# Kernel optimization log

Measured on AMD Instinct MI355X. Metric: run time of the kernel, lower is better.

## Reference

```python
import jax, jax.numpy as jnp
import numpy as np

N, K, D = 500_000, 256, 64  # points, prototypes, feature dim


def setup_inputs() -> dict:
    key = jax.random.key(0)
    kx, km = jax.random.split(key)
    X = jax.random.normal(kx, (N, D), dtype=jnp.float32)
    mus = jax.random.normal(km, (K, D), dtype=jnp.float32)
    return {"X": X, "mus": mus}


def reference(X, mus):
    # Faithful to vmap(lambda x: argmin(sum((mus - x)**2, axis=1)))(X),
    # but expressed with the Gram-matrix distance trick so the K*D broadcast
    # is a single GEMM instead of an O(N,K,D) elementwise intermediate.
    x_sq = jnp.sum(X * X, axis=1, keepdims=True)        # [N, 1]
    mu_sq = jnp.sum(mus * mus, axis=1)                  # [K]
    d2 = x_sq - 2.0 * (X @ mus.T) + mu_sq[None, :]      # [N, K] squared dists
    return jnp.argmin(d2, axis=1)                       # [N] int assignments
```

## Files before the change

### kernel.cpp

```cpp
#include <hip/hip_runtime.h>


#define DIM 64
#define NPROTO 256
#define NBLK 1024
#define MARGIN_ACC 0.017f

using f32x4 = __attribute__((ext_vector_type(4))) float;
using f16x8 = __attribute__((ext_vector_type(8))) _Float16;

__device__ __forceinline__ f16x8 cvt8(float4 a, float4 b) {
    f16x8 r;
    r[0] = (_Float16)a.x; r[1] = (_Float16)a.y;
    r[2] = (_Float16)a.z; r[3] = (_Float16)a.w;
    r[4] = (_Float16)b.x; r[5] = (_Float16)b.y;
    r[6] = (_Float16)b.z; r[7] = (_Float16)b.w;
    return r;
}

__device__ __forceinline__ void barrier_keep_vmcnt() {
    asm volatile("s_waitcnt lgkmcnt(0)" ::: "memory");
    __builtin_amdgcn_s_barrier();
    __builtin_amdgcn_sched_barrier(0);
}

#define PACK_TREE(acc, b1, b2)                                          \
    {                                                                   \
        float pv[4];                                                    \
        _Pragma("unroll")                                               \
        for (int r = 0; r < 4; ++r) {                                   \
            unsigned u = __float_as_uint(acc[r]);                       \
            u = (u & 0xFFFFFF00u) + (unsigned)(kofs - p * 16 - r);      \
            pv[r] = __uint_as_float(u);                                 \
        }                                                               \
        const float t1a = fmaxf(pv[0], pv[1]), t2a = fminf(pv[0], pv[1]);\
        const float t1b = fmaxf(pv[2], pv[3]), t2b = fminf(pv[2], pv[3]);\
        const float p1 = fmaxf(t1a, t1b);                               \
        const float p2 = fmaxf(fminf(t1a, t1b), fmaxf(t2a, t2b));       \
        const float nb2 = fmaxf(fminf(b1, p1), fmaxf(b2, p2));          \
        b1 = fmaxf(b1, p1);                                             \
        b2 = nb2;                                                       \
    }

__attribute__((amdgpu_waves_per_eu(2, 4)))
__global__ void __launch_bounds__(128)
argmin_mfma_kernel(const float* __restrict__ X,
                   const float* __restrict__ mus,
                   int* __restrict__ out,
                   unsigned* __restrict__ ws_count,
                   int* __restrict__ ws_list,
                   int use_list, int n) {
    __shared__ __align__(16) float s_seed[NPROTO];
    __shared__ uint2 s_pair[2][32];

    const int tid = threadIdx.x;
    const int w = tid >> 6;
    const int l = tid & 63;
    const int lp = l & 15;
    const int lg = l >> 4;

    f16x8 ah[8][2];
#pragma unroll
    for (int p = 0; p < 8; ++p) {
        const float* src = mus + (size_t)(w * 128 + p * 16 + lp) * DIM + lg * 8;
        const float4 a = *(const float4*)(src);
        const float4 b = *(const float4*)(src + 4);
        const float4 c = *(const float4*)(src + 32);
        const float4 d = *(const float4*)(src + 36);
        ah[p][0] = cvt8(a, b);
        ah[p][1] = cvt8(c, d);
        float s = 0.f;
        s = fmaf(a.x, a.x, fmaf(a.y, a.y, fmaf(a.z, a.z, fmaf(a.w, a.w, s))));
        s = fmaf(b.x, b.x, fmaf(b.y, b.y, fmaf(b.z, b.z, fmaf(b.w, b.w, s))));
        s = fmaf(c.x, c.x, fmaf(c.y, c.y, fmaf(c.z, c.z, fmaf(c.w, c.w, s))));
        s = fmaf(d.x, d.x, fmaf(d.y, d.y, fmaf(d.z, d.z, fmaf(d.w, d.w, s))));
        s += __shfl_xor(s, 16);
        s += __shfl_xor(s, 32);
        if (lg == 0) s_seed[w * 128 + p * 16 + lp] = -0.5f * s;
    }
    __syncthreads();

    const int ng2 = (n + 31) / 32;
    const int q = ng2 / NBLK, rr = ng2 % NBLK;
    const int bid = blockIdx.x;
    const int g0 = bid * q + (bid < rr ? bid : rr);
    const int cnt = q + (bid < rr ? 1 : 0);

    const int kofs = 255 - w * 128 - lg * 4;
    const int sbase = w * 128 + lg * 4;

    float4 xa0, xa1, xa2, xa3, xb0, xb1, xb2, xb3;
    if (cnt > 0) {
        int rA = g0 * 32 + lp;      rA = (rA < n) ? rA : (n - 1);
        int rB = g0 * 32 + 16 + lp; rB = (rB < n) ? rB : (n - 1);
        const float* pA = X + (size_t)rA * DIM + lg * 8;
        const float* pB = X + (size_t)rB * DIM + lg * 8;
        xa0 = *(const float4*)(pA);      xa1 = *(const float4*)(pA + 4);
        xa2 = *(const float4*)(pA + 32); xa3 = *(const float4*)(pA + 36);
        xb0 = *(const float4*)(pB);      xb1 = *(const float4*)(pB + 4);
        xb2 = *(const float4*)(pB + 32); xb3 = *(const float4*)(pB + 36);
    }

    for (int it = 0; it < cnt; ++it) {
        const int g = g0 + it;
        const int par = it & 1;
        const bool more = (it + 1 < cnt);

        const f16x8 bxA0 = cvt8(xa0, xa1), bxA1 = cvt8(xa2, xa3);
        const f16x8 bxB0 = cvt8(xb0, xb1), bxB1 = cvt8(xb2, xb3);

        if (more) {
            int rA = (g + 1) * 32 + lp;      rA = (rA < n) ? rA : (n - 1);
            int rB = (g + 1) * 32 + 16 + lp; rB = (rB < n) ? rB : (n - 1);
            const float* pA = X + (size_t)rA * DIM + lg * 8;
            const float* pB = X + (size_t)rB * DIM + lg * 8;
            xa0 = *(const float4*)(pA);      xa1 = *(const float4*)(pA + 4);
            xa2 = *(const float4*)(pA + 32); xa3 = *(const float4*)(pA + 36);
            xb0 = *(const float4*)(pB);      xb1 = *(const float4*)(pB + 4);
            xb2 = *(const float4*)(pB + 32); xb3 = *(const float4*)(pB + 36);
        }

        float b1A = -3.4e38f, b2A = -3.4e38f;
        float b1B = -3.4e38f, b2B = -3.4e38f;
#pragma unroll
        for (int p = 0; p < 8; ++p) {
            const f32x4 seed = *(const f32x4*)&s_seed[sbase + p * 16];
            f32x4 accA = __builtin_amdgcn_mfma_f32_16x16x32_f16(
                ah[p][0], bxA0, seed, 0, 0, 0);
            f32x4 accB = __builtin_amdgcn_mfma_f32_16x16x32_f16(
                ah[p][0], bxB0, seed, 0, 0, 0);
            accA = __builtin_amdgcn_mfma_f32_16x16x32_f16(ah[p][1], bxA1,
                                                          accA, 0, 0, 0);
            accB = __builtin_amdgcn_mfma_f32_16x16x32_f16(ah[p][1], bxB1,
                                                          accB, 0, 0, 0);
            PACK_TREE(accA, b1A, b2A)
            PACK_TREE(accB, b1B, b2B)
        }
#pragma unroll
        for (int m = 16; m <= 32; m <<= 1) {
            const float o1A = __shfl_xor(b1A, m), o2A = __shfl_xor(b2A, m);
            const float o1B = __shfl_xor(b1B, m), o2B = __shfl_xor(b2B, m);
            const float n2A = fmaxf(fminf(b1A, o1A), fmaxf(b2A, o2A));
            const float n2B = fmaxf(fminf(b1B, o1B), fmaxf(b2B, o2B));
            b1A = fmaxf(b1A, o1A); b2A = n2A;
            b1B = fmaxf(b1B, o1B); b2B = n2B;
        }
        if (w == 1 && l < 16) {
            s_pair[par][l] = make_uint2(__float_as_uint(b1A),
                                        __float_as_uint(b2A));
            s_pair[par][16 + l] = make_uint2(__float_as_uint(b1B),
                                             __float_as_uint(b2B));
        }
        barrier_keep_vmcnt();

        bool fl = false;
        const int i = g * 32 + l;
        if (w == 0 && l < 32 && i < n) {
            float f1 = (l < 16) ? b1A : b1B;
            float f2 = (l < 16) ? b2A : b2B;
            const uint2 o = s_pair[par][l];
            const float o1 = __uint_as_float(o.x), o2 = __uint_as_float(o.y);
            const float nb2 = fmaxf(fminf(f1, o1), fmaxf(f2, o2));
            f1 = fmaxf(f1, o1);
            f2 = nb2;
            const unsigned u1 = __float_as_uint(f1);
            const int k1 = 255 - (int)(u1 & 0xFFu);
            const float v1 = __uint_as_float(u1 & 0xFFFFFF00u);
            const float v2 =
                __uint_as_float(__float_as_uint(f2) & 0xFFFFFF00u);
            const bool close = (v1 - v2) < MARGIN_ACC;
            if (use_list) {
                out[i] = k1;
                fl = close;
            } else {
                out[i] = (int)((unsigned)k1 | (close ? 0x80000000u : 0u));
            }
        }
        if (use_list) {
            const unsigned long long mask = __ballot(fl);
            if (mask) {
                unsigned base = 0;
                if (l == 0)
                    base = atomicAdd(ws_count, (unsigned)__popcll(mask));
                base = __shfl(base, 0);
                if (fl)
                    ws_list[base + __popcll(mask & ((1ull << l) - 1))] = i;
            }
        }
    }
}

#define MSTRIDE 65

__global__ void __launch_bounds__(256)
fixup_lds_kernel(const float* __restrict__ X, const float* __restrict__ mus,
                 const unsigned* __restrict__ ws_count,
                 const int* __restrict__ ws_list, int* __restrict__ out) {
    __shared__ float s_mu[NPROTO * MSTRIDE];
    __shared__ float s_msq[NPROTO];

    const int tid = threadIdx.x;
    {
        const float4* mr = (const float4*)(mus + (size_t)tid * DIM);
        float q0 = 0.f, q1 = 0.f, q2 = 0.f, q3 = 0.f;
#pragma unroll
        for (int qq = 0; qq < 16; ++qq) {
            const float4 mv = mr[qq];
            const int base = tid * MSTRIDE + qq * 4;
            s_mu[base]     = mv.x;
            s_mu[base + 1] = mv.y;
            s_mu[base + 2] = mv.z;
            s_mu[base + 3] = mv.w;
            q0 = fmaf(mv.x, mv.x, q0);
            q1 = fmaf(mv.y, mv.y, q1);
            q2 = fmaf(mv.z, mv.z, q2);
            q3 = fmaf(mv.w, mv.w, q3);
        }
        s_msq[tid] = (q0 + q1) + (q2 + q3);
    }
    __syncthreads();

    const int l = tid & 63;
    const int gw = (int)((blockIdx.x * blockDim.x + tid) >> 6);
    const int NW = (int)((gridDim.x * blockDim.x) >> 6);
    const int nf = (int)*ws_count;

    for (int j = gw; j < nf; j += NW) {
        const int pt = ws_list[j];
        const float4* xr = (const float4*)(X + (size_t)pt * DIM);
        float4 xv[16];
        float a0 = 0.f, a1 = 0.f, a2 = 0.f, a3 = 0.f;
#pragma unroll
        for (int qq = 0; qq < 16; ++qq) {
            xv[qq] = xr[qq];
            a0 = fmaf(xv[qq].x, xv[qq].x, a0);
            a1 = fmaf(xv[qq].y, xv[qq].y, a1);
            a2 = fmaf(xv[qq].z, xv[qq].z, a2);
            a3 = fmaf(xv[qq].w, xv[qq].w, a3);
        }
        const float xsq = (a0 + a1) + (a2 + a3);
        float b1 = 3.4e38f;
        int k1 = 0;
#pragma unroll
        for (int e = 0; e < 4; ++e) {
            const int p = e * 64 + l;
            const float* mr = &s_mu[p * MSTRIDE];
            float d0 = 0.f, d1 = 0.f, d2 = 0.f, d3 = 0.f;
#pragma unroll
            for (int qq = 0; qq < 16; ++qq) {
                d0 = fmaf(mr[qq * 4],     xv[qq].x, d0);
                d1 = fmaf(mr[qq * 4 + 1], xv[qq].y, d1);
                d2 = fmaf(mr[qq * 4 + 2], xv[qq].z, d2);
                d3 = fmaf(mr[qq * 4 + 3], xv[qq].w, d3);
            }
            const float dot = (d0 + d1) + (d2 + d3);
            const float dd = (xsq - 2.0f * dot) + s_msq[p];
            if (dd < b1) { b1 = dd; k1 = p; }
        }
#pragma unroll
        for (int mm = 1; mm < 64; mm <<= 1) {
            const float ob = __shfl_xor(b1, mm);
            const int ok = __shfl_xor(k1, mm);
            if (ob < b1 || (ob == b1 && ok < k1)) { b1 = ob; k1 = ok; }
        }
        if (l == 0) out[pt] = k1;
    }
}

__device__ __forceinline__ int recompute_point(const float* __restrict__ X,
                                               const float* __restrict__ mus,
                                               int pt, int l) {
    const float4* xr = (const float4*)(X + (size_t)pt * DIM);
    float4 xv[16];
    float xa0 = 0.f, xa1 = 0.f, xa2 = 0.f, xa3 = 0.f;
#pragma unroll
    for (int qq = 0; qq < 16; ++qq) {
        xv[qq] = xr[qq];
        xa0 = fmaf(xv[qq].x, xv[qq].x, xa0);
        xa1 = fmaf(xv[qq].y, xv[qq].y, xa1);
        xa2 = fmaf(xv[qq].z, xv[qq].z, xa2);
        xa3 = fmaf(xv[qq].w, xv[qq].w, xa3);
    }
    const float xsq = (xa0 + xa1) + (xa2 + xa3);
    float b1 = 3.4e38f; int k1 = 0;
#pragma unroll
    for (int e = 0; e < 4; ++e) {
        const int p = l * 4 + e;
        const float4* mr = (const float4*)(mus + (size_t)p * DIM);
        float d0 = 0.f, d1 = 0.f, d2a = 0.f, d3 = 0.f;
        float q0 = 0.f, q1 = 0.f, q2 = 0.f, q3 = 0.f;
#pragma unroll
        for (int qq = 0; qq < 16; ++qq) {
            const float4 mv = mr[qq];
            d0 = fmaf(mv.x, xv[qq].x, d0);
            d1 = fmaf(mv.y, xv[qq].y, d1);
            d2a = fmaf(mv.z, xv[qq].z, d2a);
            d3 = fmaf(mv.w, xv[qq].w, d3);
            q0 = fmaf(mv.x, mv.x, q0);
            q1 = fmaf(mv.y, mv.y, q1);
            q2 = fmaf(mv.z, mv.z, q2);
            q3 = fmaf(mv.w, mv.w, q3);
        }
        const float dot = (d0 + d1) + (d2a + d3);
        const float msq = (q0 + q1) + (q2 + q3);
        const float dd = (xsq - 2.0f * dot) + msq;
        if (dd < b1) { b1 = dd; k1 = p; }
    }
#pragma unroll
    for (int mm = 1; mm < 64; mm <<= 1) {
        const float ob = __shfl_xor(b1, mm);
        const int ok = __shfl_xor(k1, mm);
        if (ob < b1 || (ob == b1 && ok < k1)) { b1 = ob; k1 = ok; }
    }
    return k1;
}

__global__ void __launch_bounds__(256)
fixup_scan_kernel(const float* __restrict__ X, const float* __restrict__ mus,
                  int* __restrict__ out, int n) {
    const int gw = (int)((blockIdx.x * blockDim.x + threadIdx.x) >> 6);
    const int l = threadIdx.x & 63;
    const int NW = (int)((gridDim.x * blockDim.x) >> 6);
    const int chunk = (n + NW - 1) / NW;
    const int base = gw * chunk;
    const int end = (base + chunk < n) ? (base + chunk) : n;
    for (int s = base; s < end; s += 64) {
        const int i = s + l;
        const int v = (i < end) ? out[i] : 0;
        const bool flg = (i < end) && ((unsigned)v & 0x80000000u);
        unsigned long long m = __ballot(flg);
        while (m) {
            const int src = (int)__ffsll((unsigned long long)m) - 1;
            m &= m - 1;
            const int pt = __shfl(i, src);
            const int k1 = recompute_point(X, mus, pt, l);
            if (l == 0) out[pt] = k1;
        }
    }
}

extern "C" void kernel_launch(void* const* d_in, const int* in_sizes, int n_in,
                              void* d_out, int out_size, void* d_ws, size_t ws_size,
                              hipStream_t stream) {
    const float* X = (const float*)d_in[0];
    const float* mus = (const float*)d_in[1];
    int* out = (int*)d_out;
    const int n = in_sizes[0] / DIM;

    unsigned* ws_count = (unsigned*)d_ws;
    int* ws_list = (int*)((char*)d_ws + 16);
    const int use_list = (ws_size >= 16 + (size_t)n * 4) ? 1 : 0;

    if (use_list) {
        hipMemsetAsync(d_ws, 0, 16, stream);
    }

    argmin_mfma_kernel<<<NBLK, 128, 0, stream>>>(X, mus, out, ws_count,
                                                 ws_list, use_list, n);
    if (use_list) {
        fixup_lds_kernel<<<512, 256, 0, stream>>>(X, mus, ws_count, ws_list,
                                                  out);
    } else {
        fixup_scan_kernel<<<512, 256, 0, stream>>>(X, mus, out, n);
    }
}
```

Before: 77.28 us.

## Unroll main loop by two with double-buffered X prefetch and drop atomic fixup list

```diff
diff --git a/kernel.cpp b/kernel.cpp
--- a/kernel.cpp
+++ b/kernel.cpp
@@ -42,16 +42,88 @@
         b2 = nb2;                                                       \
     }
 
+#define LOADX(gt, x0, x1, x2, x3, y0, y1, y2, y3)                       \
+    {                                                                   \
+        int rA_ = (gt) * 32 + lp;      rA_ = (rA_ < n) ? rA_ : (n - 1); \
+        int rB_ = (gt) * 32 + 16 + lp; rB_ = (rB_ < n) ? rB_ : (n - 1); \
+        const float* pA_ = X + (size_t)rA_ * DIM + lg * 8;              \
+        const float* pB_ = X + (size_t)rB_ * DIM + lg * 8;              \
+        x0 = *(const float4*)(pA_);      x1 = *(const float4*)(pA_ + 4);\
+        x2 = *(const float4*)(pA_ + 32); x3 = *(const float4*)(pA_ + 36);\
+        y0 = *(const float4*)(pB_);      y1 = *(const float4*)(pB_ + 4);\
+        y2 = *(const float4*)(pB_ + 32); y3 = *(const float4*)(pB_ + 36);\
+    }
+
+#define BODY(gcur, gnext, PAR, x0, x1, x2, x3, y0, y1, y2, y3)          \
+    {                                                                   \
+        const f16x8 bxA0 = cvt8(x0, x1), bxA1 = cvt8(x2, x3);           \
+        const f16x8 bxB0 = cvt8(y0, y1), bxB1 = cvt8(y2, y3);           \
+        LOADX(gnext, x0, x1, x2, x3, y0, y1, y2, y3)                    \
+        float b1A = -3.4e38f, b2A = -3.4e38f;                           \
+        float b1B = -3.4e38f, b2B = -3.4e38f;                           \
+        _Pragma("unroll")                                               \
+        for (int p = 0; p < 8; ++p) {                                   \
+            const f32x4 seed = *(const f32x4*)&s_seed[sbase + p * 16];  \
+            f32x4 accA = __builtin_amdgcn_mfma_f32_16x16x32_f16(        \
+                ah[p][0], bxA0, seed, 0, 0, 0);                         \
+            f32x4 accB = __builtin_amdgcn_mfma_f32_16x16x32_f16(        \
+                ah[p][0], bxB0, seed, 0, 0, 0);                         \
+            accA = __builtin_amdgcn_mfma_f32_16x16x32_f16(              \
+                ah[p][1], bxA1, accA, 0, 0, 0);                         \
+            accB = __builtin_amdgcn_mfma_f32_16x16x32_f16(              \
+                ah[p][1], bxB1, accB, 0, 0, 0);                         \
+            PACK_TREE(accA, b1A, b2A)                                   \
+            PACK_TREE(accB, b1B, b2B)                                   \
+        }                                                               \
+        _Pragma("unroll")                                               \
+        for (int m = 16; m <= 32; m <<= 1) {                            \
+            const float o1A = __shfl_xor(b1A, m), o2A = __shfl_xor(b2A, m);\
+            const float o1B = __shfl_xor(b1B, m), o2B = __shfl_xor(b2B, m);\
+            const float n2A = fmaxf(fminf(b1A, o1A), fmaxf(b2A, o2A));  \
+            const float n2B = fmaxf(fminf(b1B, o1B), fmaxf(b2B, o2B));  \
+            b1A = fmaxf(b1A, o1A); b2A = n2A;                           \
+            b1B = fmaxf(b1B, o1B); b2B = n2B;                           \
+        }                                                               \
+         \
+         \
+        if (w == 0 && l >= 16 && l < 32)                                \
+            s_pair[PAR][0][l] = make_uint2(__float_as_uint(b1B),        \
+                                           __float_as_uint(b2B));       \
+        if (w == 1 && l < 16)                                           \
+            s_pair[PAR][1][l] = make_uint2(__float_as_uint(b1A),        \
+                                           __float_as_uint(b2A));       \
+        barrier_keep_vmcnt();                                           \
+        const bool mine = (w == 0) ? (l < 16) : (l >= 16 && l < 32);    \
+        if (mine) {                                                     \
+            float f1 = (l < 16) ? b1A : b1B;                            \
+            float f2 = (l < 16) ? b2A : b2B;                            \
+            const uint2 o = s_pair[PAR][1 - w][l];                      \
+            const float o1 = __uint_as_float(o.x);                      \
+            const float o2 = __uint_as_float(o.y);                      \
+            const float nb2 = fmaxf(fminf(f1, o1), fmaxf(f2, o2));      \
+            f1 = fmaxf(f1, o1);                                         \
+            f2 = nb2;                                                   \
+            const int i = (gcur) * 32 + l;                              \
+            if (i < n) {                                                \
+                const unsigned u1 = __float_as_uint(f1);                \
+                const int k1 = 255 - (int)(u1 & 0xFFu);                 \
+                const float v1 = __uint_as_float(u1 & 0xFFFFFF00u);     \
+                const float v2 =                                        \
+                    __uint_as_float(__float_as_uint(f2) & 0xFFFFFF00u); \
+                const unsigned fb =                                     \
+                    ((v1 - v2) < MARGIN_ACC) ? 0x80000000u : 0u;        \
+                out[i] = (int)((unsigned)k1 | fb);                      \
+            }                                                           \
+        }                                                               \
+    }
+
 __attribute__((amdgpu_waves_per_eu(2, 4)))
 __global__ void __launch_bounds__(128)
 argmin_mfma_kernel(const float* __restrict__ X,
                    const float* __restrict__ mus,
-                   int* __restrict__ out,
-                   unsigned* __restrict__ ws_count,
-                   int* __restrict__ ws_list,
-                   int use_list, int n) {
+                   int* __restrict__ out, int n) {
     __shared__ __align__(16) float s_seed[NPROTO];
-    __shared__ uint2 s_pair[2][32];
+    __shared__ uint2 s_pair[2][2][32];
 
     const int tid = threadIdx.x;
     const int w = tid >> 6;
@@ -85,117 +157,40 @@
     const int bid = blockIdx.x;
     const int g0 = bid * q + (bid < rr ? bid : rr);
     const int cnt = q + (bid < rr ? 1 : 0);
+    const int glast = g0 + cnt - 1;
 
     const int kofs = 255 - w * 128 - lg * 4;
     const int sbase = w * 128 + lg * 4;
 
-    float4 xa0, xa1, xa2, xa3, xb0, xb1, xb2, xb3;
-    if (cnt > 0) {
-        int rA = g0 * 32 + lp;      rA = (rA < n) ? rA : (n - 1);
-        int rB = g0 * 32 + 16 + lp; rB = (rB < n) ? rB : (n - 1);
-        const float* pA = X + (size_t)rA * DIM + lg * 8;
-        const float* pB = X + (size_t)rB * DIM + lg * 8;
-        xa0 = *(const float4*)(pA);      xa1 = *(const float4*)(pA + 4);
-        xa2 = *(const float4*)(pA + 32); xa3 = *(const float4*)(pA + 36);
-        xb0 = *(const float4*)(pB);      xb1 = *(const float4*)(pB + 4);
-        xb2 = *(const float4*)(pB + 32); xb3 = *(const float4*)(pB + 36);
-    }
-
-    for (int it = 0; it < cnt; ++it) {
-        const int g = g0 + it;
-        const int par = it & 1;
-        const bool more = (it + 1 < cnt);
-
-        const f16x8 bxA0 = cvt8(xa0, xa1), bxA1 = cvt8(xa2, xa3);
-        const f16x8 bxB0 = cvt8(xb0, xb1), bxB1 = cvt8(xb2, xb3);
-
-        if (more) {
-            int rA = (g + 1) * 32 + lp;      rA = (rA < n) ? rA : (n - 1);
-            int rB = (g + 1) * 32 + 16 + lp; rB = (rB < n) ? rB : (n - 1);
-            const float* pA = X + (size_t)rA * DIM + lg * 8;
-            const float* pB = X + (size_t)rB * DIM + lg * 8;
-            xa0 = *(const float4*)(pA);      xa1 = *(const float4*)(pA + 4);
-            xa2 = *(const float4*)(pA + 32); xa3 = *(const float4*)(pA + 36);
-            xb0 = *(const float4*)(pB);      xb1 = *(const float4*)(pB + 4);
-            xb2 = *(const float4*)(pB + 32); xb3 = *(const float4*)(pB + 36);
-        }
-
-        float b1A = -3.4e38f, b2A = -3.4e38f;
-        float b1B = -3.4e38f, b2B = -3.4e38f;
-#pragma unroll
-        for (int p = 0; p < 8; ++p) {
-            const f32x4 seed = *(const f32x4*)&s_seed[sbase + p * 16];
-            f32x4 accA = __builtin_amdgcn_mfma_f32_16x16x32_f16(
-                ah[p][0], bxA0, seed, 0, 0, 0);
-            f32x4 accB = __builtin_amdgcn_mfma_f32_16x16x32_f16(
-                ah[p][0], bxB0, seed, 0, 0, 0);
-            accA = __builtin_amdgcn_mfma_f32_16x16x32_f16(ah[p][1], bxA1,
-                                                          accA, 0, 0, 0);
-            accB = __builtin_amdgcn_mfma_f32_16x16x32_f16(ah[p][1], bxB1,
-                                                          accB, 0, 0, 0);
-            PACK_TREE(accA, b1A, b2A)
-            PACK_TREE(accB, b1B, b2B)
-        }
-#pragma unroll
-        for (int m = 16; m <= 32; m <<= 1) {
-            const float o1A = __shfl_xor(b1A, m), o2A = __shfl_xor(b2A, m);
-            const float o1B = __shfl_xor(b1B, m), o2B = __shfl_xor(b2B, m);
-            const float n2A = fmaxf(fminf(b1A, o1A), fmaxf(b2A, o2A));
-            const float n2B = fmaxf(fminf(b1B, o1B), fmaxf(b2B, o2B));
-            b1A = fmaxf(b1A, o1A); b2A = n2A;
-            b1B = fmaxf(b1B, o1B); b2B = n2B;
-        }
-        if (w == 1 && l < 16) {
-            s_pair[par][l] = make_uint2(__float_as_uint(b1A),
-                                        __float_as_uint(b2A));
-            s_pair[par][16 + l] = make_uint2(__float_as_uint(b1B),
-                                             __float_as_uint(b2B));
-        }
-        barrier_keep_vmcnt();
-
-        bool fl = false;
-        const int i = g * 32 + l;
-        if (w == 0 && l < 32 && i < n) {
-            float f1 = (l < 16) ? b1A : b1B;
-            float f2 = (l < 16) ? b2A : b2B;
-            const uint2 o = s_pair[par][l];
-            const float o1 = __uint_as_float(o.x), o2 = __uint_as_float(o.y);
-            const float nb2 = fmaxf(fminf(f1, o1), fmaxf(f2, o2));
-            f1 = fmaxf(f1, o1);
-            f2 = nb2;
-            const unsigned u1 = __float_as_uint(f1);
-            const int k1 = 255 - (int)(u1 & 0xFFu);
-            const float v1 = __uint_as_float(u1 & 0xFFFFFF00u);
-            const float v2 =
-                __uint_as_float(__float_as_uint(f2) & 0xFFFFFF00u);
-            const bool close = (v1 - v2) < MARGIN_ACC;
-            if (use_list) {
-                out[i] = k1;
-                fl = close;
-            } else {
-                out[i] = (int)((unsigned)k1 | (close ? 0x80000000u : 0u));
-            }
-        }
-        if (use_list) {
-            const unsigned long long mask = __ballot(fl);
-            if (mask) {
-                unsigned base = 0;
-                if (l == 0)
-                    base = atomicAdd(ws_count, (unsigned)__popcll(mask));
-                base = __shfl(base, 0);
-                if (fl)
-                    ws_list[base + __popcll(mask & ((1ull << l) - 1))] = i;
-            }
-        }
+    float4 pa0, pa1, pa2, pa3, pb0, pb1, pb2, pb3;
+    float4 qa0, qa1, qa2, qa3, qb0, qb1, qb2, qb3;
+    LOADX(g0, pa0, pa1, pa2, pa3, pb0, pb1, pb2, pb3)
+    {
+        const int g1 = (g0 + 1 < glast) ? (g0 + 1) : glast;
+        LOADX(g1, qa0, qa1, qa2, qa3, qb0, qb1, qb2, qb3)
+    }
+
+    int it = 0;
+    for (; it + 1 < cnt; it += 2) {
+        const int gA = g0 + it;
+        const int gB = g0 + it + 1;
+        const int nA = (gA + 2 < glast) ? (gA + 2) : glast;
+        const int nB = (gB + 2 < glast) ? (gB + 2) : glast;
+        BODY(gA, nA, 0, pa0, pa1, pa2, pa3, pb0, pb1, pb2, pb3)
+        BODY(gB, nB, 1, qa0, qa1, qa2, qa3, qb0, qb1, qb2, qb3)
+    }
+    if (it < cnt) {
+        const int gA = g0 + it;
+        BODY(gA, glast, 0, pa0, pa1, pa2, pa3, pb0, pb1, pb2, pb3)
     }
 }
 
 #define MSTRIDE 65
 
 __global__ void __launch_bounds__(256)
-fixup_lds_kernel(const float* __restrict__ X, const float* __restrict__ mus,
-                 const unsigned* __restrict__ ws_count,
-                 const int* __restrict__ ws_list, int* __restrict__ out) {
+fixup_scan_lds_kernel(const float* __restrict__ X,
+                      const float* __restrict__ mus,
+                      int* __restrict__ out, int n) {
     __shared__ float s_mu[NPROTO * MSTRIDE];
     __shared__ float s_msq[NPROTO];
 
@@ -223,107 +218,10 @@
     const int l = tid & 63;
     const int gw = (int)((blockIdx.x * blockDim.x + tid) >> 6);
     const int NW = (int)((gridDim.x * blockDim.x) >> 6);
-    const int nf = (int)*ws_count;
-
-    for (int j = gw; j < nf; j += NW) {
-        const int pt = ws_list[j];
-        const float4* xr = (const float4*)(X + (size_t)pt * DIM);
-        float4 xv[16];
-        float a0 = 0.f, a1 = 0.f, a2 = 0.f, a3 = 0.f;
-#pragma unroll
-        for (int qq = 0; qq < 16; ++qq) {
-            xv[qq] = xr[qq];
-            a0 = fmaf(xv[qq].x, xv[qq].x, a0);
-            a1 = fmaf(xv[qq].y, xv[qq].y, a1);
-            a2 = fmaf(xv[qq].z, xv[qq].z, a2);
-            a3 = fmaf(xv[qq].w, xv[qq].w, a3);
-        }
-        const float xsq = (a0 + a1) + (a2 + a3);
-        float b1 = 3.4e38f;
-        int k1 = 0;
-#pragma unroll
-        for (int e = 0; e < 4; ++e) {
-            const int p = e * 64 + l;
-            const float* mr = &s_mu[p * MSTRIDE];
-            float d0 = 0.f, d1 = 0.f, d2 = 0.f, d3 = 0.f;
-#pragma unroll
-            for (int qq = 0; qq < 16; ++qq) {
-                d0 = fmaf(mr[qq * 4],     xv[qq].x, d0);
-                d1 = fmaf(mr[qq * 4 + 1], xv[qq].y, d1);
-                d2 = fmaf(mr[qq * 4 + 2], xv[qq].z, d2);
-                d3 = fmaf(mr[qq * 4 + 3], xv[qq].w, d3);
-            }
-            const float dot = (d0 + d1) + (d2 + d3);
-            const float dd = (xsq - 2.0f * dot) + s_msq[p];
-            if (dd < b1) { b1 = dd; k1 = p; }
-        }
-#pragma unroll
-        for (int mm = 1; mm < 64; mm <<= 1) {
-            const float ob = __shfl_xor(b1, mm);
-            const int ok = __shfl_xor(k1, mm);
-            if (ob < b1 || (ob == b1 && ok < k1)) { b1 = ob; k1 = ok; }
-        }
-        if (l == 0) out[pt] = k1;
-    }
-}
-
-__device__ __forceinline__ int recompute_point(const float* __restrict__ X,
-                                               const float* __restrict__ mus,
-                                               int pt, int l) {
-    const float4* xr = (const float4*)(X + (size_t)pt * DIM);
-    float4 xv[16];
-    float xa0 = 0.f, xa1 = 0.f, xa2 = 0.f, xa3 = 0.f;
-#pragma unroll
-    for (int qq = 0; qq < 16; ++qq) {
-        xv[qq] = xr[qq];
-        xa0 = fmaf(xv[qq].x, xv[qq].x, xa0);
-        xa1 = fmaf(xv[qq].y, xv[qq].y, xa1);
-        xa2 = fmaf(xv[qq].z, xv[qq].z, xa2);
-        xa3 = fmaf(xv[qq].w, xv[qq].w, xa3);
-    }
-    const float xsq = (xa0 + xa1) + (xa2 + xa3);
-    float b1 = 3.4e38f; int k1 = 0;
-#pragma unroll
-    for (int e = 0; e < 4; ++e) {
-        const int p = l * 4 + e;
-        const float4* mr = (const float4*)(mus + (size_t)p * DIM);
-        float d0 = 0.f, d1 = 0.f, d2a = 0.f, d3 = 0.f;
-        float q0 = 0.f, q1 = 0.f, q2 = 0.f, q3 = 0.f;
-#pragma unroll
-        for (int qq = 0; qq < 16; ++qq) {
-            const float4 mv = mr[qq];
-            d0 = fmaf(mv.x, xv[qq].x, d0);
-            d1 = fmaf(mv.y, xv[qq].y, d1);
-            d2a = fmaf(mv.z, xv[qq].z, d2a);
-            d3 = fmaf(mv.w, xv[qq].w, d3);
-            q0 = fmaf(mv.x, mv.x, q0);
-            q1 = fmaf(mv.y, mv.y, q1);
-            q2 = fmaf(mv.z, mv.z, q2);
-            q3 = fmaf(mv.w, mv.w, q3);
-        }
-        const float dot = (d0 + d1) + (d2a + d3);
-        const float msq = (q0 + q1) + (q2 + q3);
-        const float dd = (xsq - 2.0f * dot) + msq;
-        if (dd < b1) { b1 = dd; k1 = p; }
-    }
-#pragma unroll
-    for (int mm = 1; mm < 64; mm <<= 1) {
-        const float ob = __shfl_xor(b1, mm);
-        const int ok = __shfl_xor(k1, mm);
-        if (ob < b1 || (ob == b1 && ok < k1)) { b1 = ob; k1 = ok; }
-    }
-    return k1;
-}
-
-__global__ void __launch_bounds__(256)
-fixup_scan_kernel(const float* __restrict__ X, const float* __restrict__ mus,
-                  int* __restrict__ out, int n) {
-    const int gw = (int)((blockIdx.x * blockDim.x + threadIdx.x) >> 6);
-    const int l = threadIdx.x & 63;
-    const int NW = (int)((gridDim.x * blockDim.x) >> 6);
     const int chunk = (n + NW - 1) / NW;
     const int base = gw * chunk;
     const int end = (base + chunk < n) ? (base + chunk) : n;
+
     for (int s = base; s < end; s += 64) {
         const int i = s + l;
         const int v = (i < end) ? out[i] : 0;
@@ -333,7 +231,42 @@
             const int src = (int)__ffsll((unsigned long long)m) - 1;
             m &= m - 1;
             const int pt = __shfl(i, src);
-            const int k1 = recompute_point(X, mus, pt, l);
+            const float4* xr = (const float4*)(X + (size_t)pt * DIM);
+            float4 xv[16];
+            float a0 = 0.f, a1 = 0.f, a2 = 0.f, a3 = 0.f;
+#pragma unroll
+            for (int qq = 0; qq < 16; ++qq) {
+                xv[qq] = xr[qq];
+                a0 = fmaf(xv[qq].x, xv[qq].x, a0);
+                a1 = fmaf(xv[qq].y, xv[qq].y, a1);
+                a2 = fmaf(xv[qq].z, xv[qq].z, a2);
+                a3 = fmaf(xv[qq].w, xv[qq].w, a3);
+            }
+            const float xsq = (a0 + a1) + (a2 + a3);
+            float b1 = 3.4e38f;
+            int k1 = 0;
+#pragma unroll
+            for (int e = 0; e < 4; ++e) {
+                const int p = e * 64 + l;
+                const float* mr = &s_mu[p * MSTRIDE];
+                float d0 = 0.f, d1 = 0.f, d2 = 0.f, d3 = 0.f;
+#pragma unroll
+                for (int qq = 0; qq < 16; ++qq) {
+                    d0 = fmaf(mr[qq * 4],     xv[qq].x, d0);
+                    d1 = fmaf(mr[qq * 4 + 1], xv[qq].y, d1);
+                    d2 = fmaf(mr[qq * 4 + 2], xv[qq].z, d2);
+                    d3 = fmaf(mr[qq * 4 + 3], xv[qq].w, d3);
+                }
+                const float dot = (d0 + d1) + (d2 + d3);
+                const float dd = (xsq - 2.0f * dot) + s_msq[p];
+                if (dd < b1) { b1 = dd; k1 = p; }
+            }
+#pragma unroll
+            for (int mm = 1; mm < 64; mm <<= 1) {
+                const float ob = __shfl_xor(b1, mm);
+                const int ok = __shfl_xor(k1, mm);
+                if (ob < b1 || (ob == b1 && ok < k1)) { b1 = ob; k1 = ok; }
+            }
             if (l == 0) out[pt] = k1;
         }
     }
@@ -347,20 +280,6 @@
     int* out = (int*)d_out;
     const int n = in_sizes[0] / DIM;
 
-    unsigned* ws_count = (unsigned*)d_ws;
-    int* ws_list = (int*)((char*)d_ws + 16);
-    const int use_list = (ws_size >= 16 + (size_t)n * 4) ? 1 : 0;
-
-    if (use_list) {
-        hipMemsetAsync(d_ws, 0, 16, stream);
-    }
-
-    argmin_mfma_kernel<<<NBLK, 128, 0, stream>>>(X, mus, out, ws_count,
-                                                 ws_list, use_list, n);
-    if (use_list) {
-        fixup_lds_kernel<<<512, 256, 0, stream>>>(X, mus, ws_count, ws_list,
-                                                  out);
-    } else {
-        fixup_scan_kernel<<<512, 256, 0, stream>>>(X, mus, out, n);
-    }
-}
+    argmin_mfma_kernel<<<NBLK, 128, 0, stream>>>(X, mus, out, n);
+    fixup_scan_lds_kernel<<<512, 256, 0, stream>>>(X, mus, out, n);
+}
```

After: 89.74 us. 1.16x slower.
